# Kernel optimization log

Hardware: AMD Instinct MI355X
Metric: run time of the kernel (lower is better)

The kernel has to match this reference:

```python
import jax, jax.numpy as jnp
import numpy as np

MARGIN = 0.3
EPS = 1e-12


def setup_inputs() -> dict:
    key = jax.random.key(0)
    k1, k2 = jax.random.split(key)
    inputs = jax.random.normal(k1, (256, 2048), dtype=jnp.float32)
    targets = jax.random.randint(k2, (256,), 0, 32, dtype=jnp.int64)
    return {"inputs": inputs, "targets": targets}


def reference(inputs, targets):
    # Pairwise Euclidean distance matrix [n, n] via GEMM.
    sq = jnp.sum(inputs * inputs, axis=1)                      # [n]
    dist = sq[:, None] + sq[None, :] - 2.0 * (inputs @ inputs.T)
    dist = jnp.sqrt(jnp.clip(dist, EPS, None))                 # [n, n]

    same = targets[:, None] == targets[None, :]                # [n, n]
    # Triplet margin for all (anchor, positive, negative) in one broadcast.
    tri = dist[:, :, None] - dist[:, None, :] + MARGIN         # [n, n, n]
    tri = jnp.clip(tri, EPS, None)
    # Valid: same label for (a, p), different label for (a, neg).
    valid = same[:, :, None] & (~same)[:, None, :]             # [n, n, n]
    # Torch version stacks only valid triplets (dynamic shape); here we
    # return the dense [n, n, n] tensor with invalid entries zeroed.
    return jnp.where(valid, tri, 0.0)
```

## Files before the change

### kernel.cpp

```cpp
#include <hip/hip_runtime.h>
#include <hip/hip_fp16.h>

#define N 256
#define D 2048
#define MARGIN_F 0.3f
#define EPS_F 1e-12f
#define SQRT_EPS_F 1e-6f
#define KSLICES 8

typedef float v4f __attribute__((ext_vector_type(4)));
typedef short bf16x8 __attribute__((ext_vector_type(8)));

static __device__ __forceinline__ unsigned short f2bf_rne(float f) {
    union { float f; unsigned u; } v; v.f = f;
    unsigned r = v.u + 0x7fffu + ((v.u >> 16) & 1u);
    return (unsigned short)(r >> 16);
}

__global__ __launch_bounds__(256) void conv_sq_kernel(const float* __restrict__ x,
                                                      unsigned short* __restrict__ xb,
                                                      float* __restrict__ sq) {
    __shared__ float red[4];
    const int row = blockIdx.x;
    const int tid = threadIdx.x;
    const float* xr = x + (size_t)row * D + tid * 8;
    float4 v0 = *(const float4*)(xr);
    float4 v1 = *(const float4*)(xr + 4);
    float acc = v0.x * v0.x + v0.y * v0.y + v0.z * v0.z + v0.w * v0.w +
                v1.x * v1.x + v1.y * v1.y + v1.z * v1.z + v1.w * v1.w;
    union { unsigned short h[8]; uint4 u; } pk;
    pk.h[0] = f2bf_rne(v0.x); pk.h[1] = f2bf_rne(v0.y);
    pk.h[2] = f2bf_rne(v0.z); pk.h[3] = f2bf_rne(v0.w);
    pk.h[4] = f2bf_rne(v1.x); pk.h[5] = f2bf_rne(v1.y);
    pk.h[6] = f2bf_rne(v1.z); pk.h[7] = f2bf_rne(v1.w);
    *(uint4*)(xb + (size_t)row * D + tid * 8) = pk.u;
#pragma unroll
    for (int off = 32; off > 0; off >>= 1) acc += __shfl_down(acc, off, 64);
    if ((tid & 63) == 0) red[tid >> 6] = acc;
    __syncthreads();
    if (tid == 0) sq[row] = red[0] + red[1] + red[2] + red[3];
}

__global__ __launch_bounds__(256) void gram_mfma_kernel(const unsigned short* __restrict__ xb,
                                                        float* __restrict__ part) {
    const int w = threadIdx.x >> 6;
    const int l = threadIdx.x & 63;
    const int i0 = blockIdx.x * 32 + (w >> 1) * 16;
    const int j0 = blockIdx.y * 32 + (w & 1) * 16;
    const int ks = blockIdx.z;
    const int kq = (l >> 4) * 8;
    const unsigned short* pa = xb + (size_t)(i0 + (l & 15)) * D + ks * 256 + kq;
    const unsigned short* pb = xb + (size_t)(j0 + (l & 15)) * D + ks * 256 + kq;
    v4f acc = {0.f, 0.f, 0.f, 0.f};
#pragma unroll
    for (int t = 0; t < 8; ++t) {
        bf16x8 af = *(const bf16x8*)(pa + t * 32);
        bf16x8 bf = *(const bf16x8*)(pb + t * 32);
        acc = __builtin_amdgcn_mfma_f32_16x16x32_bf16(af, bf, acc, 0, 0, 0);
    }
    float* pp = part + ((size_t)(i0 + (l >> 4) * 4) * KSLICES + ks) * N + j0 + (l & 15);
#pragma unroll
    for (int r = 0; r < 4; ++r)
        pp[(size_t)r * KSLICES * N] = acc[r];
}

__global__ __launch_bounds__(256) void fused_kernel(const float* __restrict__ part,
                                                    const float* __restrict__ sq,
                                                    const int* __restrict__ targets,
                                                    float* __restrict__ out) {
    __shared__ __align__(16) float drow[N];
    __shared__ int lab[N];
    const int a = blockIdx.x;
    const int tid = threadIdx.x;
    lab[tid] = targets[tid];

    const float* pr = part + (size_t)a * (KSLICES * N);
    float dot = 0.f;
#pragma unroll
    for (int ks = 0; ks < KSLICES; ++ks)
        dot += pr[ks * N + tid];
    drow[tid] = (tid == a) ? SQRT_EPS_F
                           : sqrtf(fmaxf(sq[a] + sq[tid] - 2.f * dot, EPS_F));
    __syncthreads();

    const int la = lab[a];
    const int lane = tid & 63;
    const int pq = tid >> 6;
    const int p0 = blockIdx.y * 128 + pq * 32;

    v4f dan = *(const v4f*)(drow + lane * 4);
    v4f mb = MARGIN_F - dan;
    v4f nokv = {(lab[lane * 4 + 0] != la) ? 1.f : 0.f,
                (lab[lane * 4 + 1] != la) ? 1.f : 0.f,
                (lab[lane * 4 + 2] != la) ? 1.f : 0.f,
                (lab[lane * 4 + 3] != la) ? 1.f : 0.f};

    float* obase = out + ((size_t)a << 16) + lane * 4;
#pragma unroll 4
    for (int i = 0; i < 32; ++i) {
        int p = p0 + i;
        v4f r = {0.f, 0.f, 0.f, 0.f};
        if (lab[p] == la) {
            float dap = drow[p];
            v4f t = dap + mb;
            t.x = fmaxf(t.x, EPS_F);
            t.y = fmaxf(t.y, EPS_F);
            t.z = fmaxf(t.z, EPS_F);
            t.w = fmaxf(t.w, EPS_F);
            r = t * nokv;
        }
        *(v4f*)(obase + (size_t)p * N) = r;
    }
}

__global__ __launch_bounds__(64) void sq_kernel(const float* __restrict__ x,
                                                float* __restrict__ sq) {
    int row = blockIdx.x;
    int lane = threadIdx.x;
    const float4* xr = (const float4*)(x + (size_t)row * D);
    float acc = 0.f;
#pragma unroll
    for (int it = 0; it < 8; ++it) {
        float4 v = xr[lane + 64 * it];
        acc += v.x * v.x + v.y * v.y + v.z * v.z + v.w * v.w;
    }
#pragma unroll
    for (int off = 32; off > 0; off >>= 1) acc += __shfl_down(acc, off, 64);
    if (lane == 0) sq[row] = acc;
}

__global__ __launch_bounds__(256) void gram_valu_kernel(const float* __restrict__ x,
                                                        __half* __restrict__ part) {
    __shared__ __align__(16) float As[64 * 68];
    __shared__ __align__(16) float Bs[64 * 68];
    const int i0 = blockIdx.x * 64, j0 = blockIdx.y * 64, k0 = blockIdx.z * 64;
    const int tid = threadIdx.x;
#pragma unroll
    for (int it = 0; it < 4; ++it) {
        int f = tid + 256 * it;
        int row = f >> 4;
        int c4 = f & 15;
        int sc4 = c4 ^ ((row >> 2) & 15);
        float4 va = *(const float4*)(x + (size_t)(i0 + row) * D + k0 + c4 * 4);
        float4 vb = *(const float4*)(x + (size_t)(j0 + row) * D + k0 + c4 * 4);
        *(float4*)(As + row * 68 + sc4 * 4) = va;
        *(float4*)(Bs + row * 68 + sc4 * 4) = vb;
    }
    __syncthreads();
    const int tx = tid & 15, ty = tid >> 4;
    float acc[4][4];
#pragma unroll
    for (int r = 0; r < 4; ++r)
#pragma unroll
        for (int c = 0; c < 4; ++c) acc[r][c] = 0.f;
#pragma unroll
    for (int k4 = 0; k4 < 16; ++k4) {
        float4 a[4], b[4];
        const int ca = (k4 ^ ty) << 2, cb = (k4 ^ tx) << 2;
#pragma unroll
        for (int r = 0; r < 4; ++r) {
            a[r] = *(const float4*)(As + (ty * 4 + r) * 68 + ca);
            b[r] = *(const float4*)(Bs + (tx * 4 + r) * 68 + cb);
        }
#pragma unroll
        for (int r = 0; r < 4; ++r)
#pragma unroll
            for (int c = 0; c < 4; ++c)
                acc[r][c] += a[r].x * b[c].x + a[r].y * b[c].y +
                             a[r].z * b[c].z + a[r].w * b[c].w;
    }
    __half* pout = part + (size_t)blockIdx.z * (N * N);
#pragma unroll
    for (int r = 0; r < 4; ++r) {
        int gi = i0 + ty * 4 + r;
        union { __half2 h2[2]; uint2 u; } pk;
        pk.h2[0] = __floats2half2_rn(acc[r][0], acc[r][1]);
        pk.h2[1] = __floats2half2_rn(acc[r][2], acc[r][3]);
        *(uint2*)(pout + (size_t)gi * N + j0 + tx * 4) = pk.u;
    }
}

__global__ __launch_bounds__(256) void dist_kernel(const __half* __restrict__ part,
                                                   const float* __restrict__ sq,
                                                   float* __restrict__ dist) {
    const int a = blockIdx.x;
    const int tid = threadIdx.x;
    float dot = 0.f;
    const __half* base = part + a * N + tid;
#pragma unroll 8
    for (int ks = 0; ks < 32; ++ks)
        dot += __half2float(base[(size_t)ks * (N * N)]);
    dist[a * N + tid] = (tid == a) ? SQRT_EPS_F
                                   : sqrtf(fmaxf(sq[a] + sq[tid] - 2.f * dot, EPS_F));
}

__global__ __launch_bounds__(256) void triplet_kernel(const float* __restrict__ dist,
                                                      const int* __restrict__ targets,
                                                      float* __restrict__ out) {
    __shared__ __align__(16) float drow[N];
    __shared__ int lab[N];
    const int a = blockIdx.x;
    const int p0 = blockIdx.y * 16;
    const int tid = threadIdx.x;
    lab[tid] = targets[tid];
    drow[tid] = dist[a * N + tid];
    __syncthreads();
    const int la = lab[a];
    const int lane = tid & 63;
    const int pq = tid >> 6;
    v4f dan = *(const v4f*)(drow + lane * 4);
    v4f mb = MARGIN_F - dan;
    v4f nokv = {(lab[lane * 4 + 0] != la) ? 1.f : 0.f,
                (lab[lane * 4 + 1] != la) ? 1.f : 0.f,
                (lab[lane * 4 + 2] != la) ? 1.f : 0.f,
                (lab[lane * 4 + 3] != la) ? 1.f : 0.f};
    float* obase = out + ((size_t)a << 16) + lane * 4;
#pragma unroll
    for (int j = 0; j < 4; ++j) {
        int p = p0 + pq * 4 + j;
        v4f r = {0.f, 0.f, 0.f, 0.f};
        if (lab[p] == la) {
            float dap = drow[p];
            v4f t = dap + mb;
            t.x = fmaxf(t.x, EPS_F);
            t.y = fmaxf(t.y, EPS_F);
            t.z = fmaxf(t.z, EPS_F);
            t.w = fmaxf(t.w, EPS_F);
            r = t * nokv;
        }
        *(v4f*)(obase + (size_t)p * N) = r;
    }
}

extern "C" void kernel_launch(void* const* d_in, const int* in_sizes, int n_in,
                              void* d_out, int out_size, void* d_ws, size_t ws_size,
                              hipStream_t stream) {
    const float* x = (const float*)d_in[0];
    const int* targets = (const int*)d_in[1];
    float* out = (float*)d_out;
    float* ws = (float*)d_ws;

    float* sq = ws;
    unsigned short* xb = (unsigned short*)(ws + 256);
    float* part = (float*)(xb + (size_t)N * D);
    size_t need = 256 * 4 + (size_t)N * D * 2 + (size_t)KSLICES * N * N * 4 + 1024;

    if (ws_size >= need) {
        conv_sq_kernel<<<256, 256, 0, stream>>>(x, xb, sq);
        gram_mfma_kernel<<<dim3(8, 8, 8), 256, 0, stream>>>(xb, part);
        fused_kernel<<<dim3(256, 2), 256, 0, stream>>>(part, sq, targets, out);
    } else {
        __half* hpart = (__half*)d_out;
        float* dist = ws + 256;
        sq_kernel<<<256, 64, 0, stream>>>(x, sq);
        gram_valu_kernel<<<dim3(4, 4, 32), 256, 0, stream>>>(x, hpart);
        dist_kernel<<<256, 256, 0, stream>>>(hpart, sq, dist);
        triplet_kernel<<<dim3(256, 16), 256, 0, stream>>>(dist, targets, out);
    }
}
```

Measured before the change: 84.81 us.

## Fuse bf16 conversion into GEMM and derive squared norms from Gram diagonal

Removes the separate conversion/norm kernel: the MFMA Gram kernel now loads fp32 inputs and converts to bf16 in registers, and the diagonal-tile blocks write per-slice diagonal values as partial squared norms. The fused kernel sums those partials to get the norms. This saves one kernel launch and the bf16 staging buffer round trip. In exchange each element is loaded and converted many times across blocks, with double the load bytes, and the norms now come from bf16 products rather than fp32.

After: 85.95 us. Within noise of the previous version (+1.3%).

```diff
diff --git a/kernel.cpp b/kernel.cpp
--- a/kernel.cpp
+++ b/kernel.cpp
@@ -11,61 +11,58 @@
 typedef float v4f __attribute__((ext_vector_type(4)));
 typedef short bf16x8 __attribute__((ext_vector_type(8)));
 
-static __device__ __forceinline__ unsigned short f2bf_rne(float f) {
+static __device__ __forceinline__ short f2bf_rne(float f) {
     union { float f; unsigned u; } v; v.f = f;
     unsigned r = v.u + 0x7fffu + ((v.u >> 16) & 1u);
-    return (unsigned short)(r >> 16);
-}
-
-__global__ __launch_bounds__(256) void conv_sq_kernel(const float* __restrict__ x,
-                                                      unsigned short* __restrict__ xb,
-                                                      float* __restrict__ sq) {
-    __shared__ float red[4];
-    const int row = blockIdx.x;
-    const int tid = threadIdx.x;
-    const float* xr = x + (size_t)row * D + tid * 8;
-    float4 v0 = *(const float4*)(xr);
-    float4 v1 = *(const float4*)(xr + 4);
-    float acc = v0.x * v0.x + v0.y * v0.y + v0.z * v0.z + v0.w * v0.w +
-                v1.x * v1.x + v1.y * v1.y + v1.z * v1.z + v1.w * v1.w;
-    union { unsigned short h[8]; uint4 u; } pk;
-    pk.h[0] = f2bf_rne(v0.x); pk.h[1] = f2bf_rne(v0.y);
-    pk.h[2] = f2bf_rne(v0.z); pk.h[3] = f2bf_rne(v0.w);
-    pk.h[4] = f2bf_rne(v1.x); pk.h[5] = f2bf_rne(v1.y);
-    pk.h[6] = f2bf_rne(v1.z); pk.h[7] = f2bf_rne(v1.w);
-    *(uint4*)(xb + (size_t)row * D + tid * 8) = pk.u;
-#pragma unroll
-    for (int off = 32; off > 0; off >>= 1) acc += __shfl_down(acc, off, 64);
-    if ((tid & 63) == 0) red[tid >> 6] = acc;
-    __syncthreads();
-    if (tid == 0) sq[row] = red[0] + red[1] + red[2] + red[3];
-}
-
-__global__ __launch_bounds__(256) void gram_mfma_kernel(const unsigned short* __restrict__ xb,
-                                                        float* __restrict__ part) {
+    return (short)(r >> 16);
+}
+
+__global__ __launch_bounds__(256) void gram_mfma_kernel(const float* __restrict__ x,
+                                                        float* __restrict__ part,
+                                                        float* __restrict__ sqpart) {
     const int w = threadIdx.x >> 6;
     const int l = threadIdx.x & 63;
     const int i0 = blockIdx.x * 32 + (w >> 1) * 16;
     const int j0 = blockIdx.y * 32 + (w & 1) * 16;
     const int ks = blockIdx.z;
     const int kq = (l >> 4) * 8;
-    const unsigned short* pa = xb + (size_t)(i0 + (l & 15)) * D + ks * 256 + kq;
-    const unsigned short* pb = xb + (size_t)(j0 + (l & 15)) * D + ks * 256 + kq;
+    const float* pa = x + (size_t)(i0 + (l & 15)) * D + ks * 256 + kq;
+    const float* pb = x + (size_t)(j0 + (l & 15)) * D + ks * 256 + kq;
     v4f acc = {0.f, 0.f, 0.f, 0.f};
 #pragma unroll
     for (int t = 0; t < 8; ++t) {
-        bf16x8 af = *(const bf16x8*)(pa + t * 32);
-        bf16x8 bf = *(const bf16x8*)(pb + t * 32);
+        float4 a0 = *(const float4*)(pa + t * 32);
+        float4 a1 = *(const float4*)(pa + t * 32 + 4);
+        float4 b0 = *(const float4*)(pb + t * 32);
+        float4 b1 = *(const float4*)(pb + t * 32 + 4);
+        bf16x8 af, bf;
+        af[0] = f2bf_rne(a0.x); af[1] = f2bf_rne(a0.y);
+        af[2] = f2bf_rne(a0.z); af[3] = f2bf_rne(a0.w);
+        af[4] = f2bf_rne(a1.x); af[5] = f2bf_rne(a1.y);
+        af[6] = f2bf_rne(a1.z); af[7] = f2bf_rne(a1.w);
+        bf[0] = f2bf_rne(b0.x); bf[1] = f2bf_rne(b0.y);
+        bf[2] = f2bf_rne(b0.z); bf[3] = f2bf_rne(b0.w);
+        bf[4] = f2bf_rne(b1.x); bf[5] = f2bf_rne(b1.y);
+        bf[6] = f2bf_rne(b1.z); bf[7] = f2bf_rne(b1.w);
         acc = __builtin_amdgcn_mfma_f32_16x16x32_bf16(af, bf, acc, 0, 0, 0);
     }
     float* pp = part + ((size_t)(i0 + (l >> 4) * 4) * KSLICES + ks) * N + j0 + (l & 15);
 #pragma unroll
     for (int r = 0; r < 4; ++r)
         pp[(size_t)r * KSLICES * N] = acc[r];
+
+    if (blockIdx.x == blockIdx.y && i0 == j0) {
+        int col = l & 15;
+        int r = col - ((l >> 4) << 2);
+        if (r >= 0 && r < 4) {
+            float v = (r == 0) ? acc[0] : (r == 1) ? acc[1] : (r == 2) ? acc[2] : acc[3];
+            sqpart[ks * N + j0 + col] = v;
+        }
+    }
 }
 
 __global__ __launch_bounds__(256) void fused_kernel(const float* __restrict__ part,
-                                                    const float* __restrict__ sq,
+                                                    const float* __restrict__ sqpart,
                                                     const int* __restrict__ targets,
                                                     float* __restrict__ out) {
     __shared__ __align__(16) float drow[N];
@@ -75,12 +72,15 @@
     lab[tid] = targets[tid];
 
     const float* pr = part + (size_t)a * (KSLICES * N);
-    float dot = 0.f;
-#pragma unroll
-    for (int ks = 0; ks < KSLICES; ++ks)
+    float dot = 0.f, sqj = 0.f, sqa = 0.f;
+#pragma unroll
+    for (int ks = 0; ks < KSLICES; ++ks) {
         dot += pr[ks * N + tid];
+        sqj += sqpart[ks * N + tid];
+        sqa += sqpart[ks * N + a];
+    }
     drow[tid] = (tid == a) ? SQRT_EPS_F
-                           : sqrtf(fmaxf(sq[a] + sq[tid] - 2.f * dot, EPS_F));
+                           : sqrtf(fmaxf(sqa + sqj - 2.f * dot, EPS_F));
     __syncthreads();
 
     const int la = lab[a];
@@ -240,17 +240,16 @@
     float* out = (float*)d_out;
     float* ws = (float*)d_ws;
 
-    float* sq = ws;
-    unsigned short* xb = (unsigned short*)(ws + 256);
-    float* part = (float*)(xb + (size_t)N * D);
-    size_t need = 256 * 4 + (size_t)N * D * 2 + (size_t)KSLICES * N * N * 4 + 1024;
+    float* part = ws;
+    float* sqpart = ws + (size_t)KSLICES * N * N;
+    size_t need = (size_t)KSLICES * N * N * 4 + (size_t)KSLICES * N * 4 + 1024;
 
     if (ws_size >= need) {
-        conv_sq_kernel<<<256, 256, 0, stream>>>(x, xb, sq);
-        gram_mfma_kernel<<<dim3(8, 8, 8), 256, 0, stream>>>(xb, part);
-        fused_kernel<<<dim3(256, 2), 256, 0, stream>>>(part, sq, targets, out);
+        gram_mfma_kernel<<<dim3(8, 8, KSLICES), 256, 0, stream>>>(x, part, sqpart);
+        fused_kernel<<<dim3(256, 2), 256, 0, stream>>>(part, sqpart, targets, out);
     } else {
         __half* hpart = (__half*)d_out;
+        float* sq = ws;
         float* dist = ws + 256;
         sq_kernel<<<256, 64, 0, stream>>>(x, sq);
         gram_valu_kernel<<<dim3(4, 4, 32), 256, 0, stream>>>(x, hpart);
```
